# Performance work log

Hardware: AMD Instinct MI355X
Metric: run time of the kernel (lower is better)

## Reference

```python
import jax, jax.numpy as jnp
import numpy as np
from jax import lax


def _lstm_dir(x, W_ih, W_hh, b, reverse):
    # x: [B, T, D]; torch gate order i, f, g, o
    B, T, D = x.shape
    Hh = W_hh.shape[1]
    h0 = jnp.zeros((B, Hh), x.dtype)
    c0 = jnp.zeros((B, Hh), x.dtype)

    def step(carry, xt):
        h, c = carry
        g = xt @ W_ih.T + h @ W_hh.T + b
        i, f, gg, o = jnp.split(g, 4, axis=-1)
        c = jax.nn.sigmoid(f) * c + jax.nn.sigmoid(i) * jnp.tanh(gg)
        h = jax.nn.sigmoid(o) * jnp.tanh(c)
        return (h, c), h

    _, hs = lax.scan(step, (h0, c0), jnp.swapaxes(x, 0, 1), reverse=reverse)
    return jnp.swapaxes(hs, 0, 1)  # [B, T, Hh]


def _bilstm(x, w_ih_f, w_hh_f, b_f, w_ih_b, w_hh_b, b_b):
    fwd = _lstm_dir(x, w_ih_f, w_hh_f, b_f, reverse=False)
    bwd = _lstm_dir(x, w_ih_b, w_hh_b, b_b, reverse=True)
    return jnp.concatenate([fwd, bwd], axis=-1)


def setup_inputs() -> dict:
    key = jax.random.key(0)
    B, NS, L, H, LH, C = 8, 32, 128, 768, 256, 4
    ks = jax.random.split(key, 16)
    s = 0.05
    inp = {
        "hidden_states": jax.random.normal(ks[0], (B, NS, L, H), jnp.float32),
        "attention_mask": jax.random.randint(ks[1], (B, NS, L), 0, 2, jnp.int32),
        "wl_ih_f": jax.random.normal(ks[2], (4 * LH, H), jnp.float32) * s,
        "wl_hh_f": jax.random.normal(ks[3], (4 * LH, LH), jnp.float32) * s,
        "wl_b_f": jnp.zeros((4 * LH,), jnp.float32).at[LH:2 * LH].set(1.0),
        "wl_ih_b": jax.random.normal(ks[4], (4 * LH, H), jnp.float32) * s,
        "wl_hh_b": jax.random.normal(ks[5], (4 * LH, LH), jnp.float32) * s,
        "wl_b_b": jnp.zeros((4 * LH,), jnp.float32).at[LH:2 * LH].set(1.0),
        "ws_ih_f": jax.random.normal(ks[6], (4 * LH, 2 * LH), jnp.float32) * s,
        "ws_hh_f": jax.random.normal(ks[7], (4 * LH, LH), jnp.float32) * s,
        "ws_b_f": jnp.zeros((4 * LH,), jnp.float32).at[LH:2 * LH].set(1.0),
        "ws_ih_b": jax.random.normal(ks[8], (4 * LH, 2 * LH), jnp.float32) * s,
        "ws_hh_b": jax.random.normal(ks[9], (4 * LH, LH), jnp.float32) * s,
        "ws_b_b": jnp.zeros((4 * LH,), jnp.float32).at[LH:2 * LH].set(1.0),
        "cls_w": jax.random.uniform(ks[10], (C, 2 * LH), jnp.float32, -0.1, 0.1),
        "cls_b": jax.random.uniform(ks[11], (C,), jnp.float32, -0.1, 0.1),
    }
    return inp


def reference(hidden_states, attention_mask,
              wl_ih_f, wl_hh_f, wl_b_f, wl_ih_b, wl_hh_b, wl_b_b,
              ws_ih_f, ws_hh_f, ws_b_f, ws_ih_b, ws_hh_b, ws_b_b,
              cls_w, cls_b):
    B, NS, L, H = hidden_states.shape
    x = hidden_states.reshape(B * NS, L, H)
    m = attention_mask.reshape(B * NS, L).astype(x.dtype)

    # word-level bidirectional LSTM over each sentence
    h = _bilstm(x, wl_ih_f, wl_hh_f, wl_b_f, wl_ih_b, wl_hh_b, wl_b_b)  # [BN, L, 2LH]

    # per-sentence masked mean pooling (zeros for fully-masked sentences)
    cnt = m.sum(-1, keepdims=True)                    # [BN, 1]
    emb = jnp.einsum('btd,bt->bd', h, m) / jnp.maximum(cnt, 1.0)
    emb = jnp.where(cnt > 0, emb, 0.0)                # [BN, 2LH]
    emb = emb.reshape(B, NS, -1)

    # sentence-level bidirectional LSTM
    s = _bilstm(emb, ws_ih_f, ws_hh_f, ws_b_f, ws_ih_b, ws_hh_b, ws_b_b)  # [B, NS, 2LH]

    final = s[:, -1, :]  # dropout is identity in deterministic reference
    logits = final @ cls_w.T + cls_b
    return logits
```

## Files before the change

kernel.cpp:

```cpp
#include <hip/hip_runtime.h>
#include <math.h>


typedef __bf16 bf16x8 __attribute__((ext_vector_type(8)));
typedef float  f32x4  __attribute__((ext_vector_type(4)));

__device__ __forceinline__ float sigmoidf_(float x){ return 1.0f/(1.0f+expf(-x)); }
__device__ __forceinline__ unsigned short f2bf(float x){
    unsigned int b = __float_as_uint(x);
    b += 0x7FFFu + ((b>>16)&1u);
    return (unsigned short)(b>>16);
}
__device__ __forceinline__ float bf2f(unsigned short h){
    return __uint_as_float(((unsigned int)h)<<16);
}
__device__ __forceinline__ void split_bf(float x, unsigned short &hi, unsigned short &lo){
    hi = f2bf(x);
    lo = f2bf(x - bf2f(hi));
}
__device__ __forceinline__ uint4 pack8(const unsigned short* s){
    uint4 u;
    u.x = (unsigned)s[0] | ((unsigned)s[1]<<16);
    u.y = (unsigned)s[2] | ((unsigned)s[3]<<16);
    u.z = (unsigned)s[4] | ((unsigned)s[5]<<16);
    u.w = (unsigned)s[6] | ((unsigned)s[7]<<16);
    return u;
}

__device__ __forceinline__ void group_barrier(int* p, int members, int tid) {
    __syncthreads();
    if (tid == 0) {
        __hip_atomic_fetch_add(p, 1, __ATOMIC_RELAXED, __HIP_MEMORY_SCOPE_AGENT);
        int it = 0;
        while (__hip_atomic_load(p, __ATOMIC_RELAXED, __HIP_MEMORY_SCOPE_AGENT) < members) {
            __builtin_amdgcn_s_sleep(1);
            if (++it > (1<<22)) break;
        }
    }
    __builtin_amdgcn_fence(__ATOMIC_ACQUIRE, "workgroup");
    __syncthreads();
}

__device__ __forceinline__ unsigned tpat(int bid, int tid, int r) {
    unsigned v = (unsigned)bid * 1315423911u ^ (unsigned)tid * 2654435761u ^ 0x9E3779B9u;
    return r ? ~v : v;
}

__global__ void zero_f4(float4* __restrict__ p, int n) {
    int i = blockIdx.x * 256 + threadIdx.x;
    if (i < n) p[i] = make_float4(0.f, 0.f, 0.f, 0.f);
}

__global__ void prep_x(const float* __restrict__ X, unsigned short* __restrict__ Xsw) {
    int idx = blockIdx.x * 256 + threadIdx.x;
    int gblk = idx >> 6, ln = idx & 63;
    int mt = gblk / 24, kb = gblk - mt * 24;
    int m = mt * 16 + (ln & 15);
    int k = kb * 32 + (ln >> 4) * 8;
    const float* xp = X + (size_t)m * 768 + k;
    unsigned short hi[8], lo[8];
#pragma unroll
    for (int e = 0; e < 8; e += 4) {
        float4 v = *(const float4*)(xp + e);
        split_bf(v.x, hi[e+0], lo[e+0]);
        split_bf(v.y, hi[e+1], lo[e+1]);
        split_bf(v.z, hi[e+2], lo[e+2]);
        split_bf(v.w, hi[e+3], lo[e+3]);
    }
    *(uint4*)&Xsw[(size_t)gblk*1024 + ln*8]       = pack8(hi);
    *(uint4*)&Xsw[(size_t)gblk*1024 + 512 + ln*8] = pack8(lo);
}

__global__ void prep_wih_sw(const float* __restrict__ Wf, const float* __restrict__ Wb,
                            unsigned short* __restrict__ Wsw) {
    int idx = blockIdx.x * 256 + threadIdx.x;
    int gblk = idx >> 6, ln = idx & 63;
    int dir = gblk / 1536;
    int rem = gblk - dir * 1536;
    int ntile = rem / 24, kb = rem - ntile * 24;
    int j = ntile * 16 + (ln & 15);
    int k = kb * 32 + (ln >> 4) * 8;
    const float* wp = (dir ? Wb : Wf) + (size_t)j * 768 + k;
    unsigned short hi[8], lo[8];
#pragma unroll
    for (int e = 0; e < 8; e += 4) {
        float4 v = *(const float4*)(wp + e);
        split_bf(v.x, hi[e+0], lo[e+0]);
        split_bf(v.y, hi[e+1], lo[e+1]);
        split_bf(v.z, hi[e+2], lo[e+2]);
        split_bf(v.w, hi[e+3], lo[e+3]);
    }
    *(uint4*)&Wsw[(size_t)gblk*1024 + ln*8]       = pack8(hi);
    *(uint4*)&Wsw[(size_t)gblk*1024 + 512 + ln*8] = pack8(lo);
}

__global__ void prep_whh(const float* __restrict__ Wf, const float* __restrict__ Wb,
                         unsigned short* __restrict__ Wimg) {
    int idx = blockIdx.x * 256 + threadIdx.x;
    if (idx >= 524288) return;
    int dir = idx >> 18;
    int r   = idx & 262143;
    int u0t = r >> 14;
    int g   = (r >> 12) & 3;
    int u   = (r >> 8) & 15;
    int k   = r & 255;
    const float* W = dir ? Wb : Wf;
    float v = W[(size_t)(g*256 + u0t*16 + u) * 256 + k];
    unsigned short hi, lo; split_bf(v, hi, lo);
    size_t base = (size_t)(dir*16 + u0t) * 34816;
    Wimg[base + (g*16 + u)*264 + k]         = hi;
    Wimg[base + 16896 + (g*16 + u)*264 + k] = lo;
}

__global__ void transpose_whh(const float* __restrict__ Wf, const float* __restrict__ Wb,
                              float* __restrict__ Wt) {
    int idx = blockIdx.x * 256 + threadIdx.x;
    if (idx >= 524288) return;
    int dir = idx >> 18;
    int rem = idx & 262143;
    int k = rem >> 10;
    int j = rem & 1023;
    const float* Wp = dir ? Wb : Wf;
    Wt[idx] = Wp[j * 256 + k];
}

__global__ __launch_bounds__(256, 2) void proj_mfma(
    const unsigned short* __restrict__ Xsw,
    const unsigned short* __restrict__ Wihsw,
    const float* __restrict__ bfw, const float* __restrict__ bbw,
    float* __restrict__ Of, float* __restrict__ Ob)
{
    __shared__ unsigned short lds[24576];
    const int tid = threadIdx.x;
    const int nt = blockIdx.x;
    const int mt = blockIdx.y;
    const int sel = nt >> 3;
    const int ntl = nt & 7;
    const float* bias = sel ? bbw : bfw;
    float* Op = sel ? Ob : Of;
    const int wv = tid >> 6, ln = tid & 63;
    const int c = ln & 15, q = ln >> 4;

    f32x4 acc[4][8];
#pragma unroll
    for (int i = 0; i < 4; i++)
#pragma unroll
        for (int j = 0; j < 8; j++) acc[i][j] = f32x4{0.f,0.f,0.f,0.f};

    const unsigned short* Abase = Xsw + (size_t)(mt*16) * 24 * 1024;
    const unsigned short* Bbase = Wihsw + (size_t)(sel*64 + ntl*8) * 24 * 1024;

#pragma unroll 1
    for (int kb = 0; kb < 24; kb++) {
        __syncthreads();
#pragma unroll
        for (int jj = 0; jj < 12; jj++) {
            int cc = wv + 4*jj;
            int isB = (cc >= 32);
            int blk = isB ? ((cc - 32) >> 1) : (cc >> 1);
            int half = cc & 1;
            const unsigned short* src = (isB ? Bbase : Abase)
                                        + (size_t)(blk*24 + kb)*1024 + half*512 + ln*8;
            unsigned short* dst = lds + (isB ? 16384 : 0) + blk*1024 + half*512 + ln*8;
            __builtin_amdgcn_global_load_lds(
                (const __attribute__((address_space(1))) unsigned int*)src,
                (__attribute__((address_space(3))) unsigned int*)dst, 16, 0, 0);
        }
        __syncthreads();

        bf16x8 bhv[8], blv[8];
#pragma unroll
        for (int cb = 0; cb < 8; cb++) {
            bhv[cb] = *(const bf16x8*)&lds[16384 + cb*1024 + ln*8];
            blv[cb] = *(const bf16x8*)&lds[16384 + cb*1024 + 512 + ln*8];
        }
#pragma unroll
        for (int rb = 0; rb < 4; rb++) {
            int it = wv*4 + rb;
            bf16x8 ah = *(const bf16x8*)&lds[it*1024 + ln*8];
            bf16x8 al = *(const bf16x8*)&lds[it*1024 + 512 + ln*8];
#pragma unroll
            for (int cb = 0; cb < 8; cb++) {
                acc[rb][cb] = __builtin_amdgcn_mfma_f32_16x16x32_bf16(ah, bhv[cb], acc[rb][cb], 0,0,0);
                acc[rb][cb] = __builtin_amdgcn_mfma_f32_16x16x32_bf16(ah, blv[cb], acc[rb][cb], 0,0,0);
                acc[rb][cb] = __builtin_amdgcn_mfma_f32_16x16x32_bf16(al, bhv[cb], acc[rb][cb], 0,0,0);
            }
        }
    }

#pragma unroll
    for (int rb = 0; rb < 4; rb++) {
        int mbase = mt*256 + (wv*4 + rb)*16 + q*4;
#pragma unroll
        for (int cb = 0; cb < 8; cb++) {
            int j = ntl*128 + cb*16 + c;
            float bv = bias[j];
#pragma unroll
            for (int reg = 0; reg < 4; reg++) {
                int m = mbase + reg;
                int tt = m & 127, nn = m >> 7;
                Op[(size_t)(tt*256 + nn)*1024 + j] = acc[rb][cb][reg] + bv;
            }
        }
    }
}

__global__ __launch_bounds__(256, 1) void word_recur(
    const float* __restrict__ Gf, const float* __restrict__ Gb,
    const unsigned short* __restrict__ Wimg,
    unsigned short* __restrict__ hA, unsigned short* __restrict__ hB,
    const int* __restrict__ mask,
    float* __restrict__ pooled, int* __restrict__ cnt,
    int* __restrict__ pf, unsigned int* __restrict__ tstg)
{
    extern __shared__ char ldsbuf[];
    unsigned short* Hl = (unsigned short*)ldsbuf;
    float* gex   = (float*)(ldsbuf + 36864);
    int*   mk_lds= (int*)(ldsbuf + 46080);

    const int tid = threadIdx.x;
    const int bid = blockIdx.x;
    const int dir = (bid >> 3) & 1;
    const int nt  = bid & 7;
    const int u0t = bid >> 4;
    const int grp = bid & 15;
    const float* G = dir ? Gb : Gf;

    const int wv = tid >> 6, ln = tid & 63;
    const int c = ln & 15, q = ln >> 4;

    int* mycnt = cnt + grp * 136;

    bool fast;
    {
        unsigned* tl  = (unsigned*)ldsbuf;
        int* oks = (int*)(ldsbuf + 4096);
        int okl = 1;
#pragma unroll 1
        for (int r = 0; r < 2; r++) {
            __hip_atomic_store(&tstg[bid*256 + tid], tpat(bid, tid, r),
                               __ATOMIC_RELAXED, __HIP_MEMORY_SCOPE_AGENT);
            group_barrier(mycnt + 127 + 2*r, 16, tid);
            {
                int pbid = grp + 16*((u0t + 1 + wv) & 15);
                __builtin_amdgcn_global_load_lds(
                    (const __attribute__((address_space(1))) unsigned int*)
                        ((const char*)(tstg + pbid*256) + ln*16),
                    (__attribute__((address_space(3))) unsigned int*)(ldsbuf + wv*1024),
                    16, 0, 0x11 );
            }
            __syncthreads();
#pragma unroll
            for (int w2 = 0; w2 < 4; w2++) {
                int pb2 = grp + 16*((u0t + 1 + w2) & 15);
                okl &= (tl[w2*256 + tid] == tpat(pb2, tid, r)) ? 1 : 0;
            }
            group_barrier(mycnt + 128 + 2*r, 16, tid);
        }
        oks[tid] = okl;
        __syncthreads();
        if (tid == 0) {
            int o = 1;
            for (int i = 0; i < 256; i++) o &= oks[i];
            __hip_atomic_store(&pf[bid], o, __ATOMIC_RELAXED, __HIP_MEMORY_SCOPE_AGENT);
        }
        group_barrier(mycnt + 131, 16, tid);
        int f = 1;
#pragma unroll 1
        for (int k = 0; k < 16; k++)
            f &= __hip_atomic_load(&pf[grp + 16*k],
                                   __ATOMIC_RELAXED, __HIP_MEMORY_SCOPE_AGENT);
        fast = (f != 0);
    }

    {
        const char* msrc = (const char*)(mask + nt*32*128);
#pragma unroll
        for (int j = 0; j < 4; j++) {
            int i = wv + 4*j;
            __builtin_amdgcn_global_load_lds(
                (const __attribute__((address_space(1))) unsigned int*)(msrc + i*1024 + ln*16),
                (__attribute__((address_space(3))) unsigned int*)(((char*)mk_lds) + i*1024), 16, 0, 0);
        }
    }
    const unsigned short* wbase = Wimg + (size_t)(dir*16 + u0t) * 34816;
    bf16x8 wh_[8], wlo[8];
#pragma unroll
    for (int kb = 0; kb < 8; kb++) {
        wh_[kb] = *(const bf16x8*)&wbase[(wv*16 + c)*264 + kb*32 + q*8];
        wlo[kb] = *(const bf16x8*)&wbase[16896 + (wv*16 + c)*264 + kb*32 + q*8];
    }

    const int nl  = tid >> 3;
    const int up  = tid & 7;
    const int u0  = up*2;
    const int ug0 = u0t*16 + u0;
    const int n   = nt*32 + nl;

    float c0 = 0.f, c1 = 0.f, p0 = 0.f, p1 = 0.f;

    float2 gp[4];
    {
        const int te0 = dir ? 127 : 0;
        const float* Ga = G + (size_t)(te0*256 + n)*1024 + ug0;
#pragma unroll
        for (int g = 0; g < 4; g++) gp[g] = *(const float2*)&Ga[g*256];
    }

#pragma unroll 1
    for (int t = 0; t < 128; ++t) {
        const int te = dir ? (127 - t) : t;
        const unsigned short* hin = (t & 1) ? hB : hA;
        unsigned short* hout = ((t & 1) ? hA : hB) + (size_t)(dir*8 + nt) * 18432;

        if (fast) {
            const char* hsrc = (const char*)(hin + (size_t)(dir*8 + nt) * 18432);
#pragma unroll
            for (int j = 0; j < 9; j++) {
                int i = wv + 4*j;
                __builtin_amdgcn_global_load_lds(
                    (const __attribute__((address_space(1))) unsigned int*)(hsrc + i*1024 + ln*16),
                    (__attribute__((address_space(3))) unsigned int*)(ldsbuf + i*1024),
                    16, 0, 0x11 );
            }
        } else {
            const unsigned long long* hsrc =
                (const unsigned long long*)(hin + (size_t)(dir*8 + nt) * 18432);
            unsigned long long* hdst = (unsigned long long*)ldsbuf;
#pragma unroll
            for (int j = 0; j < 18; j++) {
                unsigned long long v = __hip_atomic_load(hsrc + tid + 256*j,
                        __ATOMIC_RELAXED, __HIP_MEMORY_SCOPE_AGENT);
                hdst[tid + 256*j] = v;
            }
        }
        __syncthreads();

        f32x4 acc[2];
        acc[0] = f32x4{0.f,0.f,0.f,0.f};
        acc[1] = f32x4{0.f,0.f,0.f,0.f};
#pragma unroll
        for (int kb = 0; kb < 8; kb++) {
#pragma unroll
            for (int sb = 0; sb < 2; sb++) {
                bf16x8 bh = *(const bf16x8*)&Hl[(sb*16 + c)*264 + kb*32 + q*8];
                bf16x8 bl = *(const bf16x8*)&Hl[8448 + (sb*16 + c)*264 + kb*32 + q*8];
                acc[sb] = __builtin_amdgcn_mfma_f32_16x16x32_bf16(wh_[kb], bh, acc[sb], 0, 0, 0);
                acc[sb] = __builtin_amdgcn_mfma_f32_16x16x32_bf16(wh_[kb], bl, acc[sb], 0, 0, 0);
                acc[sb] = __builtin_amdgcn_mfma_f32_16x16x32_bf16(wlo[kb], bh, acc[sb], 0, 0, 0);
            }
        }
#pragma unroll
        for (int sb = 0; sb < 2; sb++)
#pragma unroll
            for (int reg = 0; reg < 4; reg++)
                gex[(wv*16 + q*4 + reg)*36 + sb*16 + c] = acc[sb][reg];
        __syncthreads();

        float2 gpn[4];
        if (t < 127) {
            const int te1 = dir ? (126 - t) : (t + 1);
            const float* Ga = G + (size_t)(te1*256 + n)*1024 + ug0;
#pragma unroll
            for (int g = 0; g < 4; g++) gpn[g] = *(const float2*)&Ga[g*256];
        }

        const int mk = mk_lds[nl*128 + te];
        float iv0 = gex[(0*16 + u0)*36 + nl] + gp[0].x;
        float fv0 = gex[(1*16 + u0)*36 + nl] + gp[1].x;
        float gv0 = gex[(2*16 + u0)*36 + nl] + gp[2].x;
        float ov0 = gex[(3*16 + u0)*36 + nl] + gp[3].x;
        float iv1 = gex[(0*16 + u0+1)*36 + nl] + gp[0].y;
        float fv1 = gex[(1*16 + u0+1)*36 + nl] + gp[1].y;
        float gv1 = gex[(2*16 + u0+1)*36 + nl] + gp[2].y;
        float ov1 = gex[(3*16 + u0+1)*36 + nl] + gp[3].y;
        float cn0 = sigmoidf_(fv0)*c0 + sigmoidf_(iv0)*tanhf(gv0);
        float hn0 = sigmoidf_(ov0)*tanhf(cn0);
        float cn1 = sigmoidf_(fv1)*c1 + sigmoidf_(iv1)*tanhf(gv1);
        float hn1 = sigmoidf_(ov1)*tanhf(cn1);
        c0 = cn0; c1 = cn1;
        if (mk) { p0 += hn0; p1 += hn1; }
        if (t != 127) {
            unsigned short h0h, h0l, h1h, h1l;
            split_bf(hn0, h0h, h0l);
            split_bf(hn1, h1h, h1l);
            unsigned int dhi = (unsigned)h0h | ((unsigned)h1h << 16);
            unsigned int dlo = (unsigned)h0l | ((unsigned)h1l << 16);
            unsigned int* hw = (unsigned int*)hout;
            __hip_atomic_store(&hw[nl*132 + u0t*8 + up], dhi,
                               __ATOMIC_RELAXED, __HIP_MEMORY_SCOPE_AGENT);
            __hip_atomic_store(&hw[4224 + nl*132 + u0t*8 + up], dlo,
                               __ATOMIC_RELAXED, __HIP_MEMORY_SCOPE_AGENT);
        }

        if (t < 127) {
            group_barrier(mycnt + t, 16, tid);
#pragma unroll
            for (int g = 0; g < 4; g++) gp[g] = gpn[g];
        }
    }

    int cntN = 0;
#pragma unroll 1
    for (int te2 = 0; te2 < 128; ++te2) cntN += mk_lds[nl*128 + te2];
    float inv = 1.0f / fmaxf((float)cntN, 1.0f);
    *(float2*)&pooled[n*512 + dir*256 + ug0] = make_float2(p0*inv, p1*inv);
}

__global__ __launch_bounds__(256) void word_step_mfma(
    const float* __restrict__ Gf, const float* __restrict__ Gb,
    const unsigned short* __restrict__ Wimg,
    const unsigned short* __restrict__ hin_img,
    unsigned short* __restrict__ hout_img,
    const int* __restrict__ mask,
    float* __restrict__ c_st, float* __restrict__ pooled, int t)
{
    extern __shared__ char ldsbuf[];
    unsigned short* Wl = (unsigned short*)ldsbuf;
    unsigned short* Hl = Wl + 34816;
    float* gex = (float*)(ldsbuf + 69632 + 36864);

    const int tid = threadIdx.x;
    const int bid = blockIdx.x;
    const int dir = bid >> 7;
    const int u0t = (bid >> 3) & 15;
    const int nt  = bid & 7;
    const int te  = dir ? (127 - t) : t;
    const float* G = dir ? Gb : Gf;

    const int wv = tid >> 6, ln = tid & 63;
    const int c = ln & 15, q = ln >> 4;

    {
        const char* wsrc = (const char*)(Wimg + (size_t)(dir*16 + u0t) * 34816);
        const char* hsrc = (const char*)(hin_img + (size_t)(dir*8 + nt) * 18432);
        char* wdst = (char*)Wl;
        char* hdst = (char*)Hl;
#pragma unroll
        for (int j = 0; j < 17; j++) {
            int i = wv + 4*j;
            __builtin_amdgcn_global_load_lds(
                (const __attribute__((address_space(1))) unsigned int*)(wsrc + i*1024 + ln*16),
                (__attribute__((address_space(3))) unsigned int*)(wdst + i*1024), 16, 0, 0);
        }
#pragma unroll
        for (int j = 0; j < 9; j++) {
            int i = wv + 4*j;
            __builtin_amdgcn_global_load_lds(
                (const __attribute__((address_space(1))) unsigned int*)(hsrc + i*1024 + ln*16),
                (__attribute__((address_space(3))) unsigned int*)(hdst + i*1024), 16, 0, 0);
        }
    }

    const int uu = tid & 15;
    const int np = tid >> 4;
    const int uglob = u0t*16 + uu;
    const int n_a = nt*32 + np*2;
    float gpre[8]; int mk0, mk1; float cold0, cold1, pold0, pold1;
    {
        const float* Ga = G + (size_t)(te*256 + n_a)*1024 + uglob;
        const float* Gc = Ga + 1024;
#pragma unroll
        for (int g = 0; g < 4; g++) { gpre[g] = Ga[g*256]; gpre[4+g] = Gc[g*256]; }
        mk0 = mask[n_a*128 + te];
        mk1 = mask[(n_a + 1)*128 + te];
        cold0 = c_st[dir*65536 + n_a*256 + uglob];
        cold1 = c_st[dir*65536 + (n_a + 1)*256 + uglob];
        pold0 = pooled[n_a*512 + dir*256 + uglob];
        pold1 = pooled[(n_a + 1)*512 + dir*256 + uglob];
    }
    __syncthreads();

    f32x4 acc[2];
    acc[0] = f32x4{0.f,0.f,0.f,0.f};
    acc[1] = f32x4{0.f,0.f,0.f,0.f};
#pragma unroll
    for (int kb = 0; kb < 8; kb++) {
        bf16x8 ahh = *(const bf16x8*)&Wl[(wv*16 + c)*264 + kb*32 + q*8];
        bf16x8 all_ = *(const bf16x8*)&Wl[16896 + (wv*16 + c)*264 + kb*32 + q*8];
#pragma unroll
        for (int sb = 0; sb < 2; sb++) {
            bf16x8 bh = *(const bf16x8*)&Hl[(sb*16 + c)*264 + kb*32 + q*8];
            bf16x8 bl = *(const bf16x8*)&Hl[8448 + (sb*16 + c)*264 + kb*32 + q*8];
            acc[sb] = __builtin_amdgcn_mfma_f32_16x16x32_bf16(ahh, bh, acc[sb], 0, 0, 0);
            acc[sb] = __builtin_amdgcn_mfma_f32_16x16x32_bf16(ahh, bl, acc[sb], 0, 0, 0);
            acc[sb] = __builtin_amdgcn_mfma_f32_16x16x32_bf16(all_, bh, acc[sb], 0, 0, 0);
        }
    }
#pragma unroll
    for (int sb = 0; sb < 2; sb++)
#pragma unroll
        for (int reg = 0; reg < 4; reg++)
            gex[(wv*16 + q*4 + reg)*36 + sb*16 + c] = acc[sb][reg];
    __syncthreads();

    unsigned short* hout = hout_img + (size_t)(dir*8 + nt) * 18432;
    {
        int nl = np*2;
        float iv = gex[(0*16 + uu)*36 + nl] + gpre[0];
        float fv = gex[(1*16 + uu)*36 + nl] + gpre[1];
        float gv = gex[(2*16 + uu)*36 + nl] + gpre[2];
        float ov = gex[(3*16 + uu)*36 + nl] + gpre[3];
        float cn = sigmoidf_(fv)*cold0 + sigmoidf_(iv)*tanhf(gv);
        float hn = sigmoidf_(ov)*tanhf(cn);
        c_st[dir*65536 + n_a*256 + uglob] = cn;
        unsigned short hh, hl; split_bf(hn, hh, hl);
        hout[nl*264 + uglob] = hh;
        hout[8448 + nl*264 + uglob] = hl;
        if (mk0) pooled[n_a*512 + dir*256 + uglob] = pold0 + hn;
    }
    {
        int nl = np*2 + 1;
        float iv = gex[(0*16 + uu)*36 + nl] + gpre[4];
        float fv = gex[(1*16 + uu)*36 + nl] + gpre[5];
        float gv = gex[(2*16 + uu)*36 + nl] + gpre[6];
        float ov = gex[(3*16 + uu)*36 + nl] + gpre[7];
        float cn = sigmoidf_(fv)*cold1 + sigmoidf_(iv)*tanhf(gv);
        float hn = sigmoidf_(ov)*tanhf(cn);
        c_st[dir*65536 + (n_a+1)*256 + uglob] = cn;
        unsigned short hh, hl; split_bf(hn, hh, hl);
        hout[nl*264 + uglob] = hh;
        hout[8448 + nl*264 + uglob] = hl;
        if (mk1) pooled[(n_a+1)*512 + dir*256 + uglob] = pold1 + hn;
    }
}

__global__ __launch_bounds__(256) void gemm_proj(
    const float* __restrict__ A, int M, int K,
    const float* __restrict__ Wf, const float* __restrict__ Wb,
    const float* __restrict__ bf, const float* __restrict__ bb,
    float* __restrict__ Of, float* __restrict__ Ob)
{
    __shared__ float As[16][132];
    __shared__ float Bs[16][132];
    const int t = threadIdx.x;
    const int n0 = blockIdx.x * 128;
    const int m0 = blockIdx.y * 128;
    const int sel = (n0 >= 1024);
    const float* Wp = sel ? Wb : Wf;
    const float* bp = sel ? bb : bf;
    float* Op = sel ? Ob : Of;
    const int n0d = n0 & 1023;
    const int tm = t >> 4;
    const int tn = t & 15;

    float acc[8][8];
#pragma unroll
    for (int i = 0; i < 8; i++)
#pragma unroll
        for (int j = 0; j < 8; j++) acc[i][j] = 0.f;

    for (int k0 = 0; k0 < K; k0 += 16) {
        __syncthreads();
#pragma unroll
        for (int rr = 0; rr < 2; rr++) {
            int idx = t + rr * 256;
            int row = idx >> 2, kq = idx & 3;
            float4 v = *(const float4*)&A[(size_t)(m0 + row) * K + k0 + kq * 4];
            As[kq*4+0][row] = v.x; As[kq*4+1][row] = v.y;
            As[kq*4+2][row] = v.z; As[kq*4+3][row] = v.w;
        }
#pragma unroll
        for (int rr = 0; rr < 2; rr++) {
            int idx = t + rr * 256;
            int row = idx >> 2, kq = idx & 3;
            float4 v = *(const float4*)&Wp[(size_t)(n0d + row) * K + k0 + kq * 4];
            Bs[kq*4+0][row] = v.x; Bs[kq*4+1][row] = v.y;
            Bs[kq*4+2][row] = v.z; Bs[kq*4+3][row] = v.w;
        }
        __syncthreads();
#pragma unroll
        for (int k = 0; k < 16; k++) {
            float4 a0 = *(const float4*)&As[k][tm*4];
            float4 a1 = *(const float4*)&As[k][tm*4+64];
            float4 b0 = *(const float4*)&Bs[k][tn*4];
            float4 b1 = *(const float4*)&Bs[k][tn*4+64];
            float av[8] = {a0.x,a0.y,a0.z,a0.w,a1.x,a1.y,a1.z,a1.w};
            float bv[8] = {b0.x,b0.y,b0.z,b0.w,b1.x,b1.y,b1.z,b1.w};
#pragma unroll
            for (int i = 0; i < 8; i++)
#pragma unroll
                for (int j = 0; j < 8; j++)
                    acc[i][j] += av[i] * bv[j];
        }
    }

#pragma unroll
    for (int ih = 0; ih < 2; ih++) {
#pragma unroll
        for (int i = 0; i < 4; i++) {
            int m = m0 + ih*64 + tm*4 + i;
#pragma unroll
            for (int jh = 0; jh < 2; jh++) {
                int col = n0d + jh*64 + tn*4;
                float4 bias4 = *(const float4*)&bp[col];
                float4 r;
                r.x = acc[ih*4+i][jh*4+0] + bias4.x;
                r.y = acc[ih*4+i][jh*4+1] + bias4.y;
                r.z = acc[ih*4+i][jh*4+2] + bias4.z;
                r.w = acc[ih*4+i][jh*4+3] + bias4.w;
                *(float4*)&Op[(size_t)m * 1024 + col] = r;
            }
        }
    }
}

__global__ __launch_bounds__(256) void pool_div(float* __restrict__ pooled,
                                                const int* __restrict__ mask) {
    __shared__ float red[256];
    int n = blockIdx.x, t = threadIdx.x;
    red[t] = (t < 128) ? (float)mask[n*128 + t] : 0.f;
    __syncthreads();
    for (int off = 128; off > 0; off >>= 1) {
        if (t < off) red[t] += red[t + off];
        __syncthreads();
    }
    float inv = 1.0f / fmaxf(red[0], 1.0f);
    pooled[n*512 + t] *= inv;
    pooled[n*512 + 256 + t] *= inv;
}

__global__ __launch_bounds__(256) void sent_recur(
    const float* __restrict__ Gsf, const float* __restrict__ Gsb,
    const float* __restrict__ Whf, const float* __restrict__ Whb,
    float* __restrict__ hs0, float* __restrict__ hs1,
    float* __restrict__ final_h, int* __restrict__ cnt,
    int* __restrict__ pf, unsigned int* __restrict__ tstg)
{
    extern __shared__ char sbuf[];
    float* Wlds  = (float*)sbuf;
    float* h_lds = Wlds + 128*260;
    float* part  = h_lds + 256;
    float* ex    = part + 256;

    const int tid = threadIdx.x;
    const int bid = blockIdx.x;
    const int dir = (bid >> 3) & 1;
    const int b   = bid & 7;
    const int ut  = bid >> 4;
    const int grp = bid & 15;
    const float* Gs = dir ? Gsb : Gsf;
    const float* Wh = dir ? Whb : Whf;
    const int wv = tid >> 6, ln = tid & 63;

    int* mycnt = cnt + grp * 40;

    bool fast;
    {
        unsigned* tl  = (unsigned*)sbuf;
        int* oks = (int*)(sbuf + 4096);
        int okl = 1;
#pragma unroll 1
        for (int r = 0; r < 2; r++) {
            __hip_atomic_store(&tstg[bid*256 + tid], tpat(bid, tid, r) ^ 0x5A5A5A5Au,
                               __ATOMIC_RELAXED, __HIP_MEMORY_SCOPE_AGENT);
            group_barrier(mycnt + 31 + 2*r, 8, tid);
            {
                int pbid = grp + 16*((ut + 1 + wv) & 7);
                __builtin_amdgcn_global_load_lds(
                    (const __attribute__((address_space(1))) unsigned int*)
                        ((const char*)(tstg + pbid*256) + ln*16),
                    (__attribute__((address_space(3))) unsigned int*)(sbuf + wv*1024),
                    16, 0, 0x11 );
            }
            __syncthreads();
#pragma unroll
            for (int w2 = 0; w2 < 4; w2++) {
                int pb2 = grp + 16*((ut + 1 + w2) & 7);
                okl &= (tl[w2*256 + tid] == (tpat(pb2, tid, r) ^ 0x5A5A5A5Au)) ? 1 : 0;
            }
            group_barrier(mycnt + 32 + 2*r, 8, tid);
        }
        oks[tid] = okl;
        __syncthreads();
        if (tid == 0) {
            int o = 1;
            for (int i = 0; i < 256; i++) o &= oks[i];
            __hip_atomic_store(&pf[bid], o, __ATOMIC_RELAXED, __HIP_MEMORY_SCOPE_AGENT);
        }
        group_barrier(mycnt + 35, 8, tid);
        int f = 1;
#pragma unroll 1
        for (int k = 0; k < 8; k++)
            f &= __hip_atomic_load(&pf[grp + 16*k],
                                   __ATOMIC_RELAXED, __HIP_MEMORY_SCOPE_AGENT);
        fast = (f != 0);
    }

#pragma unroll
    for (int j = 0; j < 32; j++) {
        int chunk = wv + 4*j;
        int g = chunk >> 5, u2 = chunk & 31;
        const char* src = (const char*)(Wh + (size_t)(g*256 + ut*32 + u2) * 256);
        __builtin_amdgcn_global_load_lds(
            (const __attribute__((address_space(1))) unsigned int*)(src + ln*16),
            (__attribute__((address_space(3))) unsigned int*)((char*)(Wlds + chunk*260)), 16, 0, 0);
    }

    const int jloc = tid & 127, kh = tid >> 7;
    float creg = 0.f;

#pragma unroll 1
    for (int s = 0; s < 32; ++s) {
        const int t_eff = dir ? (31 - s) : s;
        const float* hin = (s & 1) ? hs1 : hs0;
        float* hout = (s & 1) ? hs0 : hs1;

        if (fast) {
            if (wv == 0)
                __builtin_amdgcn_global_load_lds(
                    (const __attribute__((address_space(1))) unsigned int*)
                        ((const char*)(hin + dir*2048 + b*256) + ln*16),
                    (__attribute__((address_space(3))) unsigned int*)((char*)h_lds),
                    16, 0, 0x11 );
        } else if (tid < 128) {
            const unsigned long long* hp =
                (const unsigned long long*)(hin + dir*2048 + b*256);
            unsigned long long v = __hip_atomic_load(hp + tid,
                    __ATOMIC_RELAXED, __HIP_MEMORY_SCOPE_AGENT);
            *(unsigned long long*)&h_lds[tid*2] = v;
        }

        float gsv = 0.f;
        if (tid < 128)
            gsv = Gs[(size_t)(b*32 + t_eff)*1024 + (jloc >> 5)*256 + ut*32 + (jloc & 31)];

        __syncthreads();

        const float* wrow = Wlds + jloc*260 + kh*128;
        const float* hrow = h_lds + kh*128;
        float acc = 0.f;
#pragma unroll
        for (int kc = 0; kc < 32; kc++) {
            float4 w4 = *(const float4*)(wrow + kc*4);
            float4 h4 = *(const float4*)(hrow + kc*4);
            acc += w4.x*h4.x + w4.y*h4.y + w4.z*h4.z + w4.w*h4.w;
        }
        part[tid] = acc;
        __syncthreads();
        if (tid < 128)
            ex[(jloc >> 5)*33 + (jloc & 31)] = part[tid] + part[tid + 128] + gsv;
        __syncthreads();
        if (tid < 32) {
            float iv = ex[0*33 + tid];
            float fv = ex[1*33 + tid];
            float gv = ex[2*33 + tid];
            float ov = ex[3*33 + tid];
            float cn = sigmoidf_(fv)*creg + sigmoidf_(iv)*tanhf(gv);
            float hn = sigmoidf_(ov)*tanhf(cn);
            creg = cn;
            int u = ut*32 + tid;
            __hip_atomic_store((unsigned int*)&hout[dir*2048 + b*256 + u],
                               __float_as_uint(hn),
                               __ATOMIC_RELAXED, __HIP_MEMORY_SCOPE_AGENT);
            if (t_eff == 31) final_h[b*512 + dir*256 + u] = hn;
        }
        if (s < 31) group_barrier(mycnt + s, 8, tid);
    }
}

__global__ __launch_bounds__(256) void sent_step(
    const float* __restrict__ Gsf, const float* __restrict__ Gsb,
    const float* __restrict__ Wt,
    const float* __restrict__ h_in, float* __restrict__ h_out,
    float* __restrict__ c_s, float* __restrict__ final_h, int s)
{
    __shared__ float h_lds[256];
    __shared__ float part[256];
    __shared__ float ex[4][33];
    const int tid = threadIdx.x;
    const int bx = blockIdx.x;
    const int dir = bx >> 6;
    const int rb = bx & 63;
    const int b = rb >> 3;
    const int ut = rb & 7;
    const int u0 = ut * 32;
    const int t_eff = dir ? (31 - s) : s;
    const float* Gs = dir ? Gsb : Gsf;

    if (tid < 64) {
        float4 v = *(const float4*)&h_in[dir*2048 + b*256 + tid*4];
        *(float4*)&h_lds[tid*4] = v;
    }
    __syncthreads();

    const int kh = tid >> 7;
    const int rr = tid & 127;
    const int g = rr >> 5;
    const int uu = rr & 31;
    const int j = g*256 + u0 + uu;
    const float* wp = Wt + dir*262144 + kh*128*1024 + j;
    float acc = 0.f;
#pragma unroll 8
    for (int k = 0; k < 128; k++)
        acc += wp[k*1024] * h_lds[kh*128 + k];
    part[tid] = acc;
    __syncthreads();
    if (tid < 128) ex[g][uu] = part[tid] + part[tid + 128];
    __syncthreads();

    if (tid < 32) {
        int u = u0 + tid;
        size_t gb = (size_t)(b*32 + t_eff)*1024 + u;
        float iv = ex[0][tid] + Gs[gb];
        float fv = ex[1][tid] + Gs[gb + 256];
        float gv = ex[2][tid] + Gs[gb + 512];
        float ov = ex[3][tid] + Gs[gb + 768];
        int ci = dir*2048 + b*256 + u;
        float cold = c_s[ci];
        float cn = sigmoidf_(fv)*cold + sigmoidf_(iv)*tanhf(gv);
        float hn = sigmoidf_(ov)*tanhf(cn);
        c_s[ci] = cn;
        h_out[ci] = hn;
        if (t_eff == 31) final_h[b*512 + dir*256 + u] = hn;
    }
}

__global__ __launch_bounds__(256) void logits_k(const float* __restrict__ fh,
                                                const float* __restrict__ cw,
                                                const float* __restrict__ cb,
                                                float* __restrict__ out) {
    __shared__ float red[256];
    int tid = threadIdx.x;
    int o = tid >> 3;
    int b = o >> 2; int c = o & 3;
    int pp = tid & 7;
    float acc = 0.f;
    const float* fv = fh + b*512 + pp*64;
    const float* wv = cw + c*512 + pp*64;
#pragma unroll 8
    for (int e = 0; e < 64; e++) acc += fv[e]*wv[e];
    red[tid] = acc;
    __syncthreads();
    if (pp == 0) {
        float s = 0.f;
#pragma unroll
        for (int qq = 0; qq < 8; qq++) s += red[o*8 + qq];
        out[o] = s + cb[c];
    }
}

extern "C" void kernel_launch(void* const* d_in, const int* in_sizes, int n_in,
                              void* d_out, int out_size, void* d_ws, size_t ws_size,
                              hipStream_t stream) {
    const float* X       = (const float*)d_in[0];
    const int*   mask    = (const int*)d_in[1];
    const float* wl_ih_f = (const float*)d_in[2];
    const float* wl_hh_f = (const float*)d_in[3];
    const float* wl_b_f  = (const float*)d_in[4];
    const float* wl_ih_b = (const float*)d_in[5];
    const float* wl_hh_b = (const float*)d_in[6];
    const float* wl_b_b  = (const float*)d_in[7];
    const float* ws_ih_f = (const float*)d_in[8];
    const float* ws_hh_f = (const float*)d_in[9];
    const float* ws_b_f  = (const float*)d_in[10];
    const float* ws_ih_b = (const float*)d_in[11];
    const float* ws_hh_b = (const float*)d_in[12];
    const float* ws_b_b  = (const float*)d_in[13];
    const float* cls_w   = (const float*)d_in[14];
    const float* cls_b   = (const float*)d_in[15];
    float* out = (float*)d_out;
    float* w = (float*)d_ws;
    (void)in_sizes; (void)n_in; (void)out_size; (void)ws_size;

    float* Gf     = w;
    float* Gb     = Gf + 33554432;
    float* Gsf    = Gb + 33554432;
    float* Gsb    = Gsf + 262144;
    float* Wt     = Gsb + 262144;
    int*   cnt_w  = (int*)Wt;
    int*   cnt_s  = cnt_w + 2176;
    int*   pf     = cnt_s + 640;
    unsigned int* tstg = (unsigned int*)(pf + 256);
    float* finalh = Wt + 524288;
    float* pooled = finalh + 4096;
    float* c_st   = pooled + 131072;
    float* hs0    = c_st + 131072;
    float* hs1    = hs0 + 4096;
    float* cs     = hs1 + 4096;
    unsigned short* hA = (unsigned short*)(cs + 4096);
    unsigned short* hB = hA + 294912;
    unsigned short* Xsw   = hB + 294912;
    unsigned short* Wihsw = Xsw + 50331648;
    unsigned short* Wimg  = Wihsw + 3145728;

    zero_f4<<<412, 256, 0, stream>>>((float4*)pooled, 105472);
    zero_f4<<<3, 256, 0, stream>>>((float4*)cnt_w, 704);
    prep_x<<<12288, 256, 0, stream>>>(X, Xsw);
    prep_wih_sw<<<768, 256, 0, stream>>>(wl_ih_f, wl_ih_b, Wihsw);
    prep_whh<<<2048, 256, 0, stream>>>(wl_hh_f, wl_hh_b, Wimg);

    proj_mfma<<<dim3(16, 128), 256, 0, stream>>>(Xsw, Wihsw, wl_b_f, wl_b_b, Gf, Gb);

    {
        (void)hipGetLastError();
        word_recur<<<256, 256, 62464, stream>>>(Gf, Gb, Wimg, hA, hB, mask,
                                                pooled, cnt_w, pf, tstg);
        hipError_t e = hipGetLastError();
        if (e != hipSuccess) {
            hipFuncSetAttribute((const void*)word_step_mfma,
                                hipFuncAttributeMaxDynamicSharedMemorySize, 115712);
            for (int t = 0; t < 128; t++) {
                const unsigned short* hin = (t & 1) ? hB : hA;
                unsigned short* hout      = (t & 1) ? hA : hB;
                word_step_mfma<<<256, 256, 115712, stream>>>(Gf, Gb, Wimg, hin, hout,
                                                             mask, c_st, pooled, t);
            }
            pool_div<<<256, 256, 0, stream>>>(pooled, mask);
        }
    }

    gemm_proj<<<dim3(16, 2), 256, 0, stream>>>(pooled, 256, 512,
                                               ws_ih_f, ws_ih_b, ws_b_f, ws_b_b,
                                               Gsf, Gsb);

    {
        hipFuncSetAttribute((const void*)sent_recur,
                            hipFuncAttributeMaxDynamicSharedMemorySize, 135696);
        (void)hipGetLastError();
        sent_recur<<<128, 256, 135696, stream>>>(Gsf, Gsb, ws_hh_f, ws_hh_b,
                                                 hs0, hs1, finalh, cnt_s,
                                                 pf, tstg);
        hipError_t e = hipGetLastError();
        if (e != hipSuccess) {
            transpose_whh<<<2048, 256, 0, stream>>>(ws_hh_f, ws_hh_b, Wt);
            for (int s = 0; s < 32; s++) {
                float* hin  = (s & 1) ? hs1 : hs0;
                float* hout = (s & 1) ? hs0 : hs1;
                sent_step<<<128, 256, 0, stream>>>(Gsf, Gsb, Wt, hin, hout, cs, finalh, s);
            }
        }
    }

    logits_k<<<1, 256, 0, stream>>>(finalh, cls_w, cls_b, out);
}
```

Measured before the change: 956.5 us.

## Replace persistent sentence LSTM kernel with per-step launches and remap projection tiles

Removes the persistent sent_recur kernel, which used inter-block spin barriers and a startup self-test, and always runs the per-timestep sent_step launches with a transposed W_hh. It also remaps proj_mfma block indices so neighbouring blocks share M tiles differently, aiming for better cache reuse. The sentence stage is meant to avoid the persistent kernel's barrier and setup costs. In exchange it pays 32 kernel launches plus a transpose on every call.

```diff
diff --git a/kernel.cpp b/kernel.cpp
--- a/kernel.cpp
+++ b/kernel.cpp
@@ -132,10 +132,11 @@
 {
     __shared__ unsigned short lds[24576];
     const int tid = threadIdx.x;
-    const int nt = blockIdx.x;
-    const int mt = blockIdx.y;
-    const int sel = nt >> 3;
-    const int ntl = nt & 7;
+    const int d   = blockIdx.x + (blockIdx.y << 4);
+    const int mt  = ((d & 7) << 4) | ((d >> 7) & 15);
+    const int nt16 = (d >> 3) & 15;
+    const int sel = nt16 >> 3;
+    const int ntl = nt16 & 7;
     const float* bias = sel ? bbw : bfw;
     float* Op = sel ? Ob : Of;
     const int wv = tid >> 6, ln = tid & 63;
@@ -233,7 +234,7 @@
 
     bool fast;
     {
-        unsigned* tl  = (unsigned*)ldsbuf;
+        unsigned* tl = (unsigned*)ldsbuf;
         int* oks = (int*)(ldsbuf + 4096);
         int okl = 1;
 #pragma unroll 1
@@ -620,145 +621,6 @@
     pooled[n*512 + 256 + t] *= inv;
 }
 
-__global__ __launch_bounds__(256) void sent_recur(
-    const float* __restrict__ Gsf, const float* __restrict__ Gsb,
-    const float* __restrict__ Whf, const float* __restrict__ Whb,
-    float* __restrict__ hs0, float* __restrict__ hs1,
-    float* __restrict__ final_h, int* __restrict__ cnt,
-    int* __restrict__ pf, unsigned int* __restrict__ tstg)
-{
-    extern __shared__ char sbuf[];
-    float* Wlds  = (float*)sbuf;
-    float* h_lds = Wlds + 128*260;
-    float* part  = h_lds + 256;
-    float* ex    = part + 256;
-
-    const int tid = threadIdx.x;
-    const int bid = blockIdx.x;
-    const int dir = (bid >> 3) & 1;
-    const int b   = bid & 7;
-    const int ut  = bid >> 4;
-    const int grp = bid & 15;
-    const float* Gs = dir ? Gsb : Gsf;
-    const float* Wh = dir ? Whb : Whf;
-    const int wv = tid >> 6, ln = tid & 63;
-
-    int* mycnt = cnt + grp * 40;
-
-    bool fast;
-    {
-        unsigned* tl  = (unsigned*)sbuf;
-        int* oks = (int*)(sbuf + 4096);
-        int okl = 1;
-#pragma unroll 1
-        for (int r = 0; r < 2; r++) {
-            __hip_atomic_store(&tstg[bid*256 + tid], tpat(bid, tid, r) ^ 0x5A5A5A5Au,
-                               __ATOMIC_RELAXED, __HIP_MEMORY_SCOPE_AGENT);
-            group_barrier(mycnt + 31 + 2*r, 8, tid);
-            {
-                int pbid = grp + 16*((ut + 1 + wv) & 7);
-                __builtin_amdgcn_global_load_lds(
-                    (const __attribute__((address_space(1))) unsigned int*)
-                        ((const char*)(tstg + pbid*256) + ln*16),
-                    (__attribute__((address_space(3))) unsigned int*)(sbuf + wv*1024),
-                    16, 0, 0x11 );
-            }
-            __syncthreads();
-#pragma unroll
-            for (int w2 = 0; w2 < 4; w2++) {
-                int pb2 = grp + 16*((ut + 1 + w2) & 7);
-                okl &= (tl[w2*256 + tid] == (tpat(pb2, tid, r) ^ 0x5A5A5A5Au)) ? 1 : 0;
-            }
-            group_barrier(mycnt + 32 + 2*r, 8, tid);
-        }
-        oks[tid] = okl;
-        __syncthreads();
-        if (tid == 0) {
-            int o = 1;
-            for (int i = 0; i < 256; i++) o &= oks[i];
-            __hip_atomic_store(&pf[bid], o, __ATOMIC_RELAXED, __HIP_MEMORY_SCOPE_AGENT);
-        }
-        group_barrier(mycnt + 35, 8, tid);
-        int f = 1;
-#pragma unroll 1
-        for (int k = 0; k < 8; k++)
-            f &= __hip_atomic_load(&pf[grp + 16*k],
-                                   __ATOMIC_RELAXED, __HIP_MEMORY_SCOPE_AGENT);
-        fast = (f != 0);
-    }
-
-#pragma unroll
-    for (int j = 0; j < 32; j++) {
-        int chunk = wv + 4*j;
-        int g = chunk >> 5, u2 = chunk & 31;
-        const char* src = (const char*)(Wh + (size_t)(g*256 + ut*32 + u2) * 256);
-        __builtin_amdgcn_global_load_lds(
-            (const __attribute__((address_space(1))) unsigned int*)(src + ln*16),
-            (__attribute__((address_space(3))) unsigned int*)((char*)(Wlds + chunk*260)), 16, 0, 0);
-    }
-
-    const int jloc = tid & 127, kh = tid >> 7;
-    float creg = 0.f;
-
-#pragma unroll 1
-    for (int s = 0; s < 32; ++s) {
-        const int t_eff = dir ? (31 - s) : s;
-        const float* hin = (s & 1) ? hs1 : hs0;
-        float* hout = (s & 1) ? hs0 : hs1;
-
-        if (fast) {
-            if (wv == 0)
-                __builtin_amdgcn_global_load_lds(
-                    (const __attribute__((address_space(1))) unsigned int*)
-                        ((const char*)(hin + dir*2048 + b*256) + ln*16),
-                    (__attribute__((address_space(3))) unsigned int*)((char*)h_lds),
-                    16, 0, 0x11 );
-        } else if (tid < 128) {
-            const unsigned long long* hp =
-                (const unsigned long long*)(hin + dir*2048 + b*256);
-            unsigned long long v = __hip_atomic_load(hp + tid,
-                    __ATOMIC_RELAXED, __HIP_MEMORY_SCOPE_AGENT);
-            *(unsigned long long*)&h_lds[tid*2] = v;
-        }
-
-        float gsv = 0.f;
-        if (tid < 128)
-            gsv = Gs[(size_t)(b*32 + t_eff)*1024 + (jloc >> 5)*256 + ut*32 + (jloc & 31)];
-
-        __syncthreads();
-
-        const float* wrow = Wlds + jloc*260 + kh*128;
-        const float* hrow = h_lds + kh*128;
-        float acc = 0.f;
-#pragma unroll
-        for (int kc = 0; kc < 32; kc++) {
-            float4 w4 = *(const float4*)(wrow + kc*4);
-            float4 h4 = *(const float4*)(hrow + kc*4);
-            acc += w4.x*h4.x + w4.y*h4.y + w4.z*h4.z + w4.w*h4.w;
-        }
-        part[tid] = acc;
-        __syncthreads();
-        if (tid < 128)
-            ex[(jloc >> 5)*33 + (jloc & 31)] = part[tid] + part[tid + 128] + gsv;
-        __syncthreads();
-        if (tid < 32) {
-            float iv = ex[0*33 + tid];
-            float fv = ex[1*33 + tid];
-            float gv = ex[2*33 + tid];
-            float ov = ex[3*33 + tid];
-            float cn = sigmoidf_(fv)*creg + sigmoidf_(iv)*tanhf(gv);
-            float hn = sigmoidf_(ov)*tanhf(cn);
-            creg = cn;
-            int u = ut*32 + tid;
-            __hip_atomic_store((unsigned int*)&hout[dir*2048 + b*256 + u],
-                               __float_as_uint(hn),
-                               __ATOMIC_RELAXED, __HIP_MEMORY_SCOPE_AGENT);
-            if (t_eff == 31) final_h[b*512 + dir*256 + u] = hn;
-        }
-        if (s < 31) group_barrier(mycnt + s, 8, tid);
-    }
-}
-
 __global__ __launch_bounds__(256) void sent_step(
     const float* __restrict__ Gsf, const float* __restrict__ Gsb,
     const float* __restrict__ Wt,
@@ -910,26 +772,16 @@
         }
     }
 
+    transpose_whh<<<2048, 256, 0, stream>>>(ws_hh_f, ws_hh_b, Wt);
+
     gemm_proj<<<dim3(16, 2), 256, 0, stream>>>(pooled, 256, 512,
                                                ws_ih_f, ws_ih_b, ws_b_f, ws_b_b,
                                                Gsf, Gsb);
 
-    {
-        hipFuncSetAttribute((const void*)sent_recur,
-                            hipFuncAttributeMaxDynamicSharedMemorySize, 135696);
-        (void)hipGetLastError();
-        sent_recur<<<128, 256, 135696, stream>>>(Gsf, Gsb, ws_hh_f, ws_hh_b,
-                                                 hs0, hs1, finalh, cnt_s,
-                                                 pf, tstg);
-        hipError_t e = hipGetLastError();
-        if (e != hipSuccess) {
-            transpose_whh<<<2048, 256, 0, stream>>>(ws_hh_f, ws_hh_b, Wt);
-            for (int s = 0; s < 32; s++) {
-                float* hin  = (s & 1) ? hs1 : hs0;
-                float* hout = (s & 1) ? hs0 : hs1;
-                sent_step<<<128, 256, 0, stream>>>(Gsf, Gsb, Wt, hin, hout, cs, finalh, s);
-            }
-        }
+    for (int s = 0; s < 32; s++) {
+        float* hin  = (s & 1) ? hs1 : hs0;
+        float* hout = (s & 1) ? hs0 : hs1;
+        sent_step<<<128, 256, 0, stream>>>(Gsf, Gsb, Wt, hin, hout, cs, finalh, s);
     }
 
     logits_k<<<1, 256, 0, stream>>>(finalh, cls_w, cls_b, out);
```

Result: slower. 1.045 ms (+9.2%).
